# Optimization experiments

Hardware: AMD Instinct MI355X
Metric: run time of the kernel (lower is better)

The kernel has to match this reference:

```python
import jax, jax.numpy as jnp
import numpy as np

N = 100_000   # nodes
E = 3_200_000 # edges
G = 512       # graphs in batch
H = 64        # hidden dim
C = 7         # num classes


def setup_inputs() -> dict:
    key = jax.random.key(0)
    ks = jax.random.split(key, 8)
    x = jax.random.normal(ks[0], (N, 1), dtype=jnp.float32)
    edge_index = jax.random.randint(ks[1], (2, E), 0, N, dtype=jnp.int32)
    batch = jnp.sort(jax.random.randint(ks[2], (N,), 0, G, dtype=jnp.int32))
    W1 = jax.random.normal(ks[3], (1, H), dtype=jnp.float32) / np.sqrt(1.0)
    b1 = jnp.zeros((H,), jnp.float32)
    W2 = jax.random.normal(ks[4], (H, H), dtype=jnp.float32) / np.sqrt(H)
    b2 = jnp.zeros((H,), jnp.float32)
    fW1 = jax.random.normal(ks[5], (H, 32), dtype=jnp.float32) / np.sqrt(H)
    fb1 = jnp.zeros((32,), jnp.float32)
    fW2 = jax.random.normal(ks[6], (32, C), dtype=jnp.float32) / np.sqrt(32.0)
    fb2 = jnp.zeros((C,), jnp.float32)
    return {"x": x, "edge_index": edge_index, "batch": batch,
            "W1": W1, "b1": b1, "W2": W2, "b2": b2,
            "fW1": fW1, "fb1": fb1, "fW2": fW2, "fb2": fb2}


def reference(x, edge_index, batch, W1, b1, W2, b2, fW1, fb1, fW2, fb2):
    # GCNConv with self-loops and symmetric normalization (PyG defaults).
    src, dst = edge_index[0], edge_index[1]
    loop = jnp.arange(N, dtype=src.dtype)
    s = jnp.concatenate([src, loop])  # [E+N]
    d = jnp.concatenate([dst, loop])
    deg = jax.ops.segment_sum(jnp.ones(s.shape, jnp.float32), d, num_segments=N)
    dis = jnp.where(deg > 0, jax.lax.rsqrt(jnp.maximum(deg, 1.0)), 0.0)
    norm = dis[s] * dis[d]  # [E+N]

    def gcn(h, W, b):
        h = h @ W                                   # [N, out]
        msg = norm[:, None] * h[s]                  # gather + scale
        return jax.ops.segment_sum(msg, d, num_segments=N) + b

    # Dropout is identity in eval/reference mode.
    h = jax.nn.relu(gcn(x, W1, b1))
    h = jax.nn.relu(gcn(h, W2, b2))

    # global_mean_pool over graph assignment `batch`
    cnt = jax.ops.segment_sum(jnp.ones((N,), jnp.float32), batch, num_segments=G)
    pooled = jax.ops.segment_sum(h, batch, num_segments=G) / jnp.maximum(cnt, 1.0)[:, None]

    h = jax.nn.relu(pooled @ fW1 + fb1)
    return h @ fW2 + fb2  # [G, C] logits
```

## Files before the change

### kernel.cpp

```cpp
#include <hip/hip_runtime.h>

#define N_NODES 100000
#define N_EDGES 3200000
#define G_GRAPHS 512
#define HDIM 64
#define CBSH 11
#define CBN 2048
#define NCB ((N_NODES + CBN - 1) / CBN)
#define EPW 4096
#define NWG ((N_EDGES + EPW - 1) / EPW)
#define EPT (EPW / 256)
#define SPL 8
#define RTHR 512
#define WPS ((NWG + SPL - 1) / SPL)
#define MAXROWS 25

__global__ __launch_bounds__(256) void kzp(const float* __restrict__ W1,
                                           const float* __restrict__ b1,
                                           const float* __restrict__ W2,
                                           float* __restrict__ dt, int* __restrict__ meta,
                                           float* __restrict__ pw1, float* __restrict__ pb1,
                                           float* __restrict__ w2p, float* __restrict__ tabs,
                                           int* __restrict__ deg, float* __restrict__ q,
                                           float* __restrict__ pool, int* __restrict__ cnt,
                                           float* __restrict__ histA, float* __restrict__ histW) {
    int tid = threadIdx.x;
    if (blockIdx.x < 16) {
        __shared__ float ts[HDIM], srt[HDIM];
        __shared__ int isnew[HDIM], rr[HDIM], kpermS[HDIM], rankS[HDIM];
        __shared__ int ndS;
        if (tid < HDIM) {
            float w1 = W1[tid], bb = b1[tid];
            ts[tid] = (w1 != 0.f) ? (-bb / w1) : -1e30f;
        }
        __syncthreads();
        if (tid < HDIM) {
            float tj = ts[tid];
            int r = 0;
            for (int i = 0; i < HDIM; ++i) {
                float ti = ts[i];
                if (ti < tj || (ti == tj && i < tid)) r++;
            }
            rr[tid] = r;
            srt[r] = tj;
            kpermS[r] = tid;
        }
        __syncthreads();
        if (tid < HDIM) {
            int r = rr[tid];
            isnew[r] = (r == 0) || (srt[r] != srt[r - 1]);
        }
        __syncthreads();
        if (tid < HDIM) {
            int r = rr[tid];
            int didx = 0;
            for (int qq = 0; qq <= r; ++qq) didx += isnew[qq];
            didx -= 1;
            rankS[tid] = didx;
            if (blockIdx.x == 0 && isnew[r]) dt[didx] = srt[r];
        }
        if (tid == 0) {
            int nd = 0;
            for (int qq = 0; qq < HDIM; ++qq) nd += isnew[qq];
            ndS = nd;
            if (blockIdx.x == 0) {
                int nw = 0;
                for (int qq = 0; qq < HDIM; ++qq) nw |= (b1[qq] != 0.f) ? 1 : 0;
                meta[0] = nd; meta[1] = nw;
            }
        }
        __syncthreads();
        int nd = ndS;
        if (blockIdx.x == 0 && tid < HDIM) {
            int pj = kpermS[tid];
            pw1[tid] = W1[pj]; pb1[tid] = b1[pj];
        }
        int i = blockIdx.x * 256 + tid;
        if (i < HDIM * HDIM) {
            int r = i >> 6, j = i & 63;
            w2p[i] = W2[kpermS[r] * HDIM + j];
        }
        if (nd <= 6 && i < (1 + 4 * nd) * HDIM) {
            int r = i >> 6, j = i & 63;
            float acc = 0.f;
            if (r == 0) {
                for (int jj = 0; jj < HDIM; ++jj)
                    if (W1[jj] == 0.f) acc += fmaxf(b1[jj], 0.f) * W2[jj * HDIM + j];
            } else {
                int qq = (r - 1) >> 2, c = (r - 1) & 3;
                for (int jj = 0; jj < HDIM; ++jj) {
                    if (rankS[jj] != qq) continue;
                    float w1 = W1[jj], bb = b1[jj];
                    float wr = W2[jj * HDIM + j];
                    if      (c == 0 && w1 > 0.f) acc += w1 * wr;
                    else if (c == 1 && w1 < 0.f) acc += w1 * wr;
                    else if (c == 2 && w1 > 0.f) acc += bb * wr;
                    else if (c == 3 && w1 < 0.f) acc += bb * wr;
                }
            }
            tabs[i] = acc;
        }
    }
    size_t gtid = (size_t)blockIdx.x * blockDim.x + threadIdx.x;
    size_t stride = (size_t)gridDim.x * blockDim.x;
    for (size_t i = gtid; i < N_NODES; i += stride) { deg[i] = 0; q[i] = 0.f; }
    for (size_t i = gtid; i < G_GRAPHS * HDIM; i += stride) pool[i] = 0.f;
    for (size_t i = gtid; i < G_GRAPHS; i += stride) cnt[i] = 0;
    size_t nh = (size_t)7 * N_NODES;
    for (size_t i = gtid; i < nh; i += stride) { histA[i] = 0.f; histW[i] = 0.f; }
}

__global__ __launch_bounds__(256) void kB2(const int* __restrict__ src,
                                           const int* __restrict__ dst,
                                           unsigned* __restrict__ sorted,
                                           int* __restrict__ wgcnt,
                                           int* __restrict__ wgpre) {
    __shared__ int hist[NCB];
    __shared__ int basep[NCB];
    __shared__ unsigned sbuf[EPW];
    int tid = threadIdx.x;
    int w = blockIdx.x;
    int e0 = w * EPW;
    int ecnt = min(EPW, N_EDGES - e0);
    if (tid < NCB) hist[tid] = 0;
    __syncthreads();
    int dreg[EPT], sreg[EPT];
    const uint4* dst4 = reinterpret_cast<const uint4*>(dst + e0);
    const uint4* src4 = reinterpret_cast<const uint4*>(src + e0);
    #pragma unroll
    for (int t = 0; t < EPT / 4; ++t) {
        int v = t * 256 + tid;
        if (v * 4 < ecnt) {
            uint4 dv = dst4[v];
            uint4 sv = src4[v];
            int base = v * 4;
            dreg[t*4+0] = (base+0 < ecnt) ? (int)dv.x : -1;
            dreg[t*4+1] = (base+1 < ecnt) ? (int)dv.y : -1;
            dreg[t*4+2] = (base+2 < ecnt) ? (int)dv.z : -1;
            dreg[t*4+3] = (base+3 < ecnt) ? (int)dv.w : -1;
            sreg[t*4+0] = (int)sv.x; sreg[t*4+1] = (int)sv.y;
            sreg[t*4+2] = (int)sv.z; sreg[t*4+3] = (int)sv.w;
            #pragma unroll
            for (int k = 0; k < 4; ++k)
                if (dreg[t*4+k] >= 0) atomicAdd(&hist[dreg[t*4+k] >> CBSH], 1);
        } else {
            dreg[t*4+0] = dreg[t*4+1] = dreg[t*4+2] = dreg[t*4+3] = -1;
        }
    }
    __syncthreads();
    if (tid < 64) {
        int h = (tid < NCB) ? hist[tid] : 0;
        int v = h;
        #pragma unroll
        for (int off = 1; off < 64; off <<= 1) {
            int uu = __shfl_up(v, off, 64);
            if (tid >= off) v += uu;
        }
        if (tid < NCB) {
            basep[tid] = v - h;
            wgcnt[w * NCB + tid] = h;
            wgpre[w * NCB + tid] = v - h;
        }
    }
    __syncthreads();
    #pragma unroll
    for (int t = 0; t < EPT; ++t) {
        int d = dreg[t];
        if (d >= 0) {
            int b = d >> CBSH;
            int pos = atomicAdd(&basep[b], 1);
            sbuf[pos] = ((unsigned)sreg[t] << CBSH) | (unsigned)(d & (CBN - 1));
        }
    }
    __syncthreads();
    uint4* out4 = reinterpret_cast<uint4*>(sorted + e0);
    const uint4* sb4 = reinterpret_cast<const uint4*>(sbuf);
    int nv4 = ecnt >> 2;
    for (int i = tid; i < nv4; i += 256) out4[i] = sb4[i];
    for (int i = (nv4 << 2) + tid; i < ecnt; i += 256) sorted[e0 + i] = sbuf[i];
}

#define FOR_RUNS(BODY)                                                        \
    {                                                                         \
        int wv = tid >> 6, ln = tid & 63;                                     \
        int w0 = sp * WPS, w1e = min(w0 + WPS, NWG);                          \
        for (int w = w0 + wv; w < w1e; w += (RTHR / 64)) {                    \
            int st = w * EPW + wgpre[w * NCB + b];                            \
            int cb = wgcnt[w * NCB + b];                                      \
            for (int i = ln; i < cb; i += 64) { unsigned ww = sorted[st + i]; BODY } \
        }                                                                     \
    }

__global__ __launch_bounds__(RTHR) void kdeg2(const unsigned* __restrict__ sorted,
                                              const int* __restrict__ wgcnt,
                                              const int* __restrict__ wgpre,
                                              int* __restrict__ deg) {
    __shared__ int dcnt[CBN];
    int b = blockIdx.x / SPL, sp = blockIdx.x % SPL, tid = threadIdx.x;
    for (int i = tid; i < CBN; i += RTHR) dcnt[i] = 0;
    __syncthreads();
    FOR_RUNS( atomicAdd(&dcnt[ww & (CBN - 1)], 1); )
    __syncthreads();
    int nb = b * CBN;
    for (int i = tid; i < CBN; i += RTHR) {
        int c = dcnt[i];
        if (c && nb + i < N_NODES) atomicAdd(&deg[nb + i], c);
    }
}

__global__ void k2_dis(const int* __restrict__ deg, const float* __restrict__ x,
                       float* __restrict__ dis, float* __restrict__ u) {
    int n = blockIdx.x * blockDim.x + threadIdx.x;
    if (n < N_NODES) {
        float d = rsqrtf((float)(deg[n] + 1));
        dis[n] = d;
        u[n] = d * x[n];
    }
}

__global__ __launch_bounds__(RTHR) void kq3(const unsigned* __restrict__ sorted,
                                            const int* __restrict__ wgcnt,
                                            const int* __restrict__ wgpre,
                                            const float* __restrict__ u,
                                            float* __restrict__ q) {
    __shared__ float qL[CBN];
    int b = blockIdx.x / SPL, sp = blockIdx.x % SPL, tid = threadIdx.x;
    for (int i = tid; i < CBN; i += RTHR) qL[i] = 0.f;
    __syncthreads();
    FOR_RUNS( atomicAdd(&qL[ww & (CBN - 1)], u[ww >> CBSH]); )
    __syncthreads();
    int nb = b * CBN;
    for (int i = tid; i < CBN; i += RTHR) {
        float v = qL[i];
        if (v != 0.f && nb + i < N_NODES) atomicAdd(&q[nb + i], v);
    }
}

__global__ void k3b(const int* __restrict__ deg, const float* __restrict__ x,
                    const float* __restrict__ dis, const float* __restrict__ q,
                    float2* __restrict__ ad) {
    int n = blockIdx.x * blockDim.x + threadIdx.x;
    if (n < N_NODES) {
        float d = dis[n];
        ad[n] = make_float2(d * q[n] + x[n] / (float)(deg[n] + 1), d);
    }
}

__global__ __launch_bounds__(RTHR) void khist(const unsigned* __restrict__ sorted,
                                              const int* __restrict__ wgcnt,
                                              const int* __restrict__ wgpre,
                                              const float2* __restrict__ ad,
                                              const float* __restrict__ dt,
                                              const int* __restrict__ meta,
                                              float* __restrict__ histA,
                                              float* __restrict__ histW) {
    __shared__ float bA[7 * CBN];
    __shared__ float dtS[8];
    int nd = meta[0], needW = meta[1];
    if (nd > 6) return;
    int b = blockIdx.x / SPL, sp = blockIdx.x % SPL, tid = threadIdx.x;
    if (tid < 8) dtS[tid] = (tid < nd) ? dt[tid] : 3.4e38f;
    int nb = b * CBN;
    int nparts = 1 + (needW ? 1 : 0);
    for (int part = 0; part < nparts; ++part) {
        for (int i = tid; i < (nd + 1) * CBN; i += RTHR) bA[i] = 0.f;
        __syncthreads();
        FOR_RUNS(
            float2 t = ad[ww >> CBSH];
            float a = t.x;
            int k = 0;
            _Pragma("unroll")
            for (int qq = 0; qq < 6; ++qq) k += (dtS[qq] < a) ? 1 : 0;
            atomicAdd(&bA[k * CBN + (ww & (CBN - 1))], part ? t.y : t.y * a);
        )
        __syncthreads();
        float* H = part ? histW : histA;
        for (int k = 0; k <= nd; ++k)
            for (int i = tid; i < CBN; i += RTHR) {
                float v = bA[k * CBN + i];
                if (v != 0.f && nb + i < N_NODES)
                    atomicAdd(&H[(size_t)k * N_NODES + nb + i], v);
            }
        __syncthreads();
    }
}

__global__ __launch_bounds__(256) void knode(
        const float* __restrict__ histA, const float* __restrict__ histW,
        const int* __restrict__ meta, const float* __restrict__ dt,
        const float* __restrict__ tabs,
        const float* __restrict__ pw1, const float* __restrict__ pb1,
        const float* __restrict__ w2p,
        const float2* __restrict__ ad, const float* __restrict__ b2,
        const int* __restrict__ batch,
        const unsigned* __restrict__ sorted, const int* __restrict__ wgcnt,
        const int* __restrict__ wgpre,
        float* __restrict__ pool, int* __restrict__ cnt) {
    __shared__ float h2s[HDIM * 65];
    __shared__ float tabL[MAXROWS * HDIM];
    __shared__ float dtS[8];
    int tid = threadIdx.x;
    int nl = tid & 63, cg = tid >> 6;
    int n0 = blockIdx.x * 64;
    int nvalid = min(64, N_NODES - n0);
    int n = n0 + min(nl, nvalid - 1);
    int nd = meta[0], needW = meta[1];
    float2 adn = ad[n];
    float a = adn.x, d = adn.y;
    int c16 = cg * 16;

    if (nd <= 6) {
        int nrows = 1 + 4 * nd;
        for (int i = tid; i < nrows * HDIM; i += 256) tabL[i] = tabs[i];
        if (tid < nd) dtS[tid] = dt[tid];
        __syncthreads();
        float TA = 0.f, TW = 0.f;
        for (int bq = 0; bq <= nd; ++bq) {
            TA += histA[(size_t)bq * N_NODES + n];
            if (needW) TW += histW[(size_t)bq * N_NODES + n];
        }
        int k = 0;
        for (int q = 0; q < nd; ++q) k += (dtS[q] < a) ? 1 : 0;
        float z[16];
        #pragma unroll
        for (int t = 0; t < 16; ++t) z[t] = b2[c16 + t];
        float d2 = d * d;
        float cC = d * TW + d2;
        #pragma unroll
        for (int t = 0; t < 16; ++t) z[t] += cC * tabL[c16 + t];
        float run = 0.f, runW = 0.f;
        for (int q = 0; q < nd; ++q) {
            run += histA[(size_t)q * N_NODES + n];
            if (needW) runW += histW[(size_t)q * N_NODES + n];
            bool act = (q < k);
            float cWp = d * (TA - run) + (act ? d2 * a : 0.f);
            float cWm = d * run + (act ? 0.f : d2 * a);
            float cBp = d * (TW - runW) + (act ? d2 : 0.f);
            float cBm = d * runW + (act ? 0.f : d2);
            int base = (1 + 4 * q) * HDIM + c16;
            #pragma unroll
            for (int t = 0; t < 16; ++t)
                z[t] += cWp * tabL[base + t] + cWm * tabL[base + HDIM + t]
                      + cBp * tabL[base + 2 * HDIM + t] + cBm * tabL[base + 3 * HDIM + t];
        }
        #pragma unroll
        for (int t = 0; t < 16; ++t) h2s[nl * 65 + c16 + t] = fmaxf(z[t], 0.f);
    } else {
        float zz[16];
        #pragma unroll
        for (int t = 0; t < 16; ++t) zz[t] = 0.f;
        int b = n >> CBSH;
        int myld = n & (CBN - 1);
        for (int w = 0; w < NWG; ++w) {
            int st = w * EPW + wgpre[w * NCB + b];
            int cb = wgcnt[w * NCB + b];
            for (int i = 0; i < cb; ++i) {
                unsigned ww = sorted[st + i];
                if ((int)(ww & (CBN - 1)) == myld) {
                    float2 t2 = ad[ww >> CBSH];
                    #pragma unroll
                    for (int t = 0; t < 16; ++t)
                        zz[t] += t2.y * fmaxf(t2.x * pw1[c16 + t] + pb1[c16 + t], 0.f);
                }
            }
        }
        #pragma unroll
        for (int t = 0; t < 16; ++t)
            zz[t] = d * zz[t] + d * d * fmaxf(a * pw1[c16 + t] + pb1[c16 + t], 0.f);
        #pragma unroll
        for (int t = 0; t < 16; ++t) h2s[nl * 65 + c16 + t] = zz[t];
        __syncthreads();
        float z[16];
        #pragma unroll
        for (int t = 0; t < 16; ++t) z[t] = b2[c16 + t];
        for (int jj = 0; jj < HDIM; ++jj) {
            float av = h2s[nl * 65 + jj];
            #pragma unroll
            for (int t = 0; t < 16; ++t) z[t] += av * w2p[jj * HDIM + c16 + t];
        }
        __syncthreads();
        #pragma unroll
        for (int t = 0; t < 16; ++t) h2s[nl * 65 + c16 + t] = fmaxf(z[t], 0.f);
    }

    __syncthreads();
    int i0 = cg * 16, i1 = min(i0 + 16, nvalid);
    float accP = 0.f; int gcur = -1, runC = 0;
    for (int i = i0; i < i1; ++i) {
        int g = batch[n0 + i];
        float v = h2s[i * 65 + nl];
        if (g != gcur) {
            if (gcur >= 0) {
                atomicAdd(&pool[(size_t)gcur * HDIM + nl], accP);
                if (nl == 0) atomicAdd(&cnt[gcur], runC);
            }
            gcur = g; accP = 0.f; runC = 0;
        }
        accP += v; ++runC;
    }
    if (gcur >= 0) {
        atomicAdd(&pool[(size_t)gcur * HDIM + nl], accP);
        if (nl == 0) atomicAdd(&cnt[gcur], runC);
    }
}

__global__ void k7_mlp(const float* __restrict__ pool, const int* __restrict__ cnt,
                       const float* __restrict__ fW1, const float* __restrict__ fb1,
                       const float* __restrict__ fW2, const float* __restrict__ fb2,
                       float* __restrict__ out) {
    __shared__ float p[HDIM];
    __shared__ float tt[32];
    int g = blockIdx.x;
    int tid = threadIdx.x;
    float c = fmaxf((float)cnt[g], 1.f);
    p[tid] = pool[g * HDIM + tid] / c;
    __syncthreads();
    if (tid < 32) {
        float acc = fb1[tid];
        #pragma unroll
        for (int j = 0; j < HDIM; ++j) acc += p[j] * fW1[j * 32 + tid];
        tt[tid] = fmaxf(acc, 0.f);
    }
    __syncthreads();
    if (tid < 7) {
        float acc = fb2[tid];
        #pragma unroll
        for (int i = 0; i < 32; ++i) acc += tt[i] * fW2[i * 7 + tid];
        out[g * 7 + tid] = acc;
    }
}

__global__ void kf1_deg(const int* __restrict__ dst, int* __restrict__ deg) {
    int e = blockIdx.x * blockDim.x + threadIdx.x;
    if (e < N_EDGES) atomicAdd(&deg[dst[e]], 1);
}
__global__ void kf2_dis(const int* __restrict__ deg, const float* __restrict__ x,
                        float* __restrict__ dis, float* __restrict__ agg1) {
    int n = blockIdx.x * blockDim.x + threadIdx.x;
    if (n < N_NODES) {
        float d = (float)(deg[n] + 1);
        dis[n] = rsqrtf(d);
        agg1[n] = x[n] / d;
    }
}
__global__ void kf3_agg1(const int* __restrict__ src, const int* __restrict__ dst,
                         const float* __restrict__ dis, const float* __restrict__ x,
                         float* __restrict__ agg1) {
    int e = blockIdx.x * blockDim.x + threadIdx.x;
    if (e < N_EDGES) {
        int s = src[e], d = dst[e];
        atomicAdd(&agg1[d], dis[s] * dis[d] * x[s]);
    }
}
__global__ void kf4_agg2init(const float* __restrict__ agg1, const float* __restrict__ dis,
                             const float* __restrict__ W1, const float* __restrict__ b1,
                             float* __restrict__ agg2) {
    int i = blockIdx.x * blockDim.x + threadIdx.x;
    if (i < N_NODES * HDIM) {
        int n = i >> 6, j = i & 63;
        float h = fmaxf(agg1[n] * W1[j] + b1[j], 0.f);
        float r = dis[n];
        agg2[i] = r * r * h;
    }
}
__global__ void kf5_edge(const int* __restrict__ src, const int* __restrict__ dst,
                         const float* __restrict__ dis, const float* __restrict__ agg1,
                         const float* __restrict__ W1, const float* __restrict__ b1,
                         float* __restrict__ agg2) {
    int t = blockIdx.x * blockDim.x + threadIdx.x;
    int e = t >> 6, j = t & 63;
    if (e < N_EDGES) {
        int s = src[e], d = dst[e];
        float w = dis[s] * dis[d];
        float h = fmaxf(agg1[s] * W1[j] + b1[j], 0.f);
        atomicAdd(&agg2[d * HDIM + j], w * h);
    }
}
__global__ void kf6_pool(const float* __restrict__ agg2, const float* __restrict__ W2,
                         const float* __restrict__ b2, const int* __restrict__ batch,
                         float* __restrict__ pool, int* __restrict__ cnt) {
    __shared__ float w2s[HDIM * HDIM];
    int tid = threadIdx.x;
    for (int i = tid; i < HDIM * HDIM; i += blockDim.x) w2s[i] = W2[i];
    __syncthreads();
    int lane = tid & 63, wid = tid >> 6;
    int nwaves = gridDim.x * 4;
    for (int n = blockIdx.x * 4 + wid; n < N_NODES; n += nwaves) {
        float av  = agg2[n * HDIM + lane];
        float acc = b2[lane];
        #pragma unroll
        for (int k = 0; k < HDIM; ++k)
            acc += __shfl(av, k, 64) * w2s[k * HDIM + lane];
        acc = fmaxf(acc, 0.f);
        int g = batch[n];
        atomicAdd(&pool[g * HDIM + lane], acc);
        if (lane == 0) atomicAdd(&cnt[g], 1);
    }
}

extern "C" void kernel_launch(void* const* d_in, const int* in_sizes, int n_in,
                              void* d_out, int out_size, void* d_ws, size_t ws_size,
                              hipStream_t stream) {
    const float* x    = (const float*)d_in[0];
    const int*   ei   = (const int*)  d_in[1];
    const int*   batch= (const int*)  d_in[2];
    const float* W1   = (const float*)d_in[3];
    const float* b1   = (const float*)d_in[4];
    const float* W2   = (const float*)d_in[5];
    const float* b2   = (const float*)d_in[6];
    const float* fW1  = (const float*)d_in[7];
    const float* fb1  = (const float*)d_in[8];
    const float* fW2  = (const float*)d_in[9];
    const float* fb2  = (const float*)d_in[10];
    const int* src = ei;
    const int* dst = ei + N_EDGES;
    float* out = (float*)d_out;

    size_t off = 0;
    auto take = [&](size_t bytes) { size_t o = off; off = (off + bytes + 255) & ~(size_t)255; return o; };
    char* base = (char*)d_ws;
    int*     deg   = (int*)     (base + take((size_t)N_NODES * 4));
    float*   pool  = (float*)   (base + take((size_t)G_GRAPHS * HDIM * 4));
    int*     cnt   = (int*)     (base + take((size_t)G_GRAPHS * 4));
    float*   dis   = (float*)   (base + take((size_t)N_NODES * 4));
    float*   u     = (float*)   (base + take((size_t)N_NODES * 4));
    float*   q     = (float*)   (base + take((size_t)N_NODES * 4));
    float2*  ad    = (float2*)  (base + take((size_t)N_NODES * 8));
    float*   dt    = (float*)   (base + take(HDIM * 4));
    int*     meta  = (int*)     (base + take(64));
    float*   pw1   = (float*)   (base + take(HDIM * 4));
    float*   pb1   = (float*)   (base + take(HDIM * 4));
    float*   w2p   = (float*)   (base + take(HDIM * HDIM * 4));
    float*   tabs  = (float*)   (base + take((size_t)MAXROWS * HDIM * 4));
    int*     wgcnt = (int*)     (base + take((size_t)NWG * NCB * 4));
    int*     wgpre = (int*)     (base + take((size_t)NWG * NCB * 4));
    size_t sorted_off = off;
    unsigned* sorted = (unsigned*)(base + take((size_t)N_EDGES * 4));
    float*   histA = (float*)   (base + take((size_t)7 * N_NODES * 4));
    float*   histW = (float*)   (base + take((size_t)7 * N_NODES * 4));
    size_t need_fast = off;

    if (ws_size >= need_fast) {
        kzp   <<<1024, 256, 0, stream>>>(W1, b1, W2, dt, meta, pw1, pb1, w2p, tabs,
                                         deg, q, pool, cnt, histA, histW);
        kB2   <<<NWG, 256, 0, stream>>>(src, dst, sorted, wgcnt, wgpre);
        kdeg2 <<<NCB * SPL, RTHR, 0, stream>>>(sorted, wgcnt, wgpre, deg);
        k2_dis<<<(N_NODES + 255) / 256, 256, 0, stream>>>(deg, x, dis, u);
        kq3   <<<NCB * SPL, RTHR, 0, stream>>>(sorted, wgcnt, wgpre, u, q);
        k3b   <<<(N_NODES + 255) / 256, 256, 0, stream>>>(deg, x, dis, q, ad);
        khist <<<NCB * SPL, RTHR, 0, stream>>>(sorted, wgcnt, wgpre, ad, dt, meta, histA, histW);
        knode <<<(N_NODES + 63) / 64, 256, 0, stream>>>(histA, histW, meta, dt, tabs,
                                                        pw1, pb1, w2p, ad, b2, batch,
                                                        sorted, wgcnt, wgpre, pool, cnt);
        k7_mlp<<<G_GRAPHS, 64, 0, stream>>>(pool, cnt, fW1, fb1, fW2, fb2, out);
    } else {
        float* agg1 = u;
        float* agg2 = (float*)(base + sorted_off);
        hipMemsetAsync(deg, 0, (size_t)N_NODES * 4, stream);
        hipMemsetAsync(pool, 0, (size_t)G_GRAPHS * HDIM * 4 + 1024, stream);
        kf1_deg<<<(N_EDGES + 255) / 256, 256, 0, stream>>>(dst, deg);
        kf2_dis<<<(N_NODES + 255) / 256, 256, 0, stream>>>(deg, x, dis, agg1);
        kf3_agg1<<<(N_EDGES + 255) / 256, 256, 0, stream>>>(src, dst, dis, x, agg1);
        kf4_agg2init<<<(N_NODES * HDIM + 255) / 256, 256, 0, stream>>>(agg1, dis, W1, b1, agg2);
        int k5_blocks = (int)(((long long)N_EDGES * HDIM + 255) / 256);
        kf5_edge<<<k5_blocks, 256, 0, stream>>>(src, dst, dis, agg1, W1, b1, agg2);
        kf6_pool<<<2048, 256, 0, stream>>>(agg2, W2, b2, batch, pool, cnt);
        k7_mlp<<<G_GRAPHS, 64, 0, stream>>>(pool, cnt, fW1, fb1, fW2, fb2, out);
    }
}
```

Measured before the change: 134.0 us.

## Merge bucket-sort and zero/prep kernels; recompute node scalars in consumers

Folds the edge bucketing kernel and the zero-init/weight-prep kernel into one launch by partitioning block indices. It also removes two small elementwise kernels (dis/u and ad computation) by recomputing rsqrt(deg+1) and the node scalar inline in the gather loops. This cuts launch count and intermediate buffer traffic. In exchange the consumers do extra gathers (deg, x, q instead of one float2) and an rsqrt per edge.

```diff
diff --git a/kernel.cpp b/kernel.cpp
--- a/kernel.cpp
+++ b/kernel.cpp
@@ -14,8 +14,14 @@
 #define RTHR 512
 #define WPS ((NWG + SPL - 1) / SPL)
 #define MAXROWS 25
-
-__global__ __launch_bounds__(256) void kzp(const float* __restrict__ W1,
+#define ZBLK 1024
+
+__global__ __launch_bounds__(256) void kBZ(const int* __restrict__ src,
+                                           const int* __restrict__ dst,
+                                           unsigned* __restrict__ sorted,
+                                           int* __restrict__ wgcnt,
+                                           int* __restrict__ wgpre,
+                                           const float* __restrict__ W1,
                                            const float* __restrict__ b1,
                                            const float* __restrict__ W2,
                                            float* __restrict__ dt, int* __restrict__ meta,
@@ -25,7 +31,73 @@
                                            float* __restrict__ pool, int* __restrict__ cnt,
                                            float* __restrict__ histA, float* __restrict__ histW) {
     int tid = threadIdx.x;
-    if (blockIdx.x < 16) {
+    if (blockIdx.x < NWG) {
+        __shared__ int hist[NCB];
+        __shared__ int basep[NCB];
+        __shared__ unsigned sbuf[EPW];
+        int w = blockIdx.x;
+        int e0 = w * EPW;
+        int ecnt = min(EPW, N_EDGES - e0);
+        if (tid < NCB) hist[tid] = 0;
+        __syncthreads();
+        int dreg[EPT], sreg[EPT];
+        const uint4* dst4 = reinterpret_cast<const uint4*>(dst + e0);
+        const uint4* src4 = reinterpret_cast<const uint4*>(src + e0);
+        #pragma unroll
+        for (int t = 0; t < EPT / 4; ++t) {
+            int v = t * 256 + tid;
+            if (v * 4 < ecnt) {
+                uint4 dv = dst4[v];
+                uint4 sv = src4[v];
+                int base = v * 4;
+                dreg[t*4+0] = (base+0 < ecnt) ? (int)dv.x : -1;
+                dreg[t*4+1] = (base+1 < ecnt) ? (int)dv.y : -1;
+                dreg[t*4+2] = (base+2 < ecnt) ? (int)dv.z : -1;
+                dreg[t*4+3] = (base+3 < ecnt) ? (int)dv.w : -1;
+                sreg[t*4+0] = (int)sv.x; sreg[t*4+1] = (int)sv.y;
+                sreg[t*4+2] = (int)sv.z; sreg[t*4+3] = (int)sv.w;
+                #pragma unroll
+                for (int k = 0; k < 4; ++k)
+                    if (dreg[t*4+k] >= 0) atomicAdd(&hist[dreg[t*4+k] >> CBSH], 1);
+            } else {
+                dreg[t*4+0] = dreg[t*4+1] = dreg[t*4+2] = dreg[t*4+3] = -1;
+            }
+        }
+        __syncthreads();
+        if (tid < 64) {
+            int h = (tid < NCB) ? hist[tid] : 0;
+            int v = h;
+            #pragma unroll
+            for (int off = 1; off < 64; off <<= 1) {
+                int uu = __shfl_up(v, off, 64);
+                if (tid >= off) v += uu;
+            }
+            if (tid < NCB) {
+                basep[tid] = v - h;
+                wgcnt[w * NCB + tid] = h;
+                wgpre[w * NCB + tid] = v - h;
+            }
+        }
+        __syncthreads();
+        #pragma unroll
+        for (int t = 0; t < EPT; ++t) {
+            int d = dreg[t];
+            if (d >= 0) {
+                int b = d >> CBSH;
+                int pos = atomicAdd(&basep[b], 1);
+                sbuf[pos] = ((unsigned)sreg[t] << CBSH) | (unsigned)(d & (CBN - 1));
+            }
+        }
+        __syncthreads();
+        uint4* out4 = reinterpret_cast<uint4*>(sorted + e0);
+        const uint4* sb4 = reinterpret_cast<const uint4*>(sbuf);
+        int nv4 = ecnt >> 2;
+        for (int i = tid; i < nv4; i += 256) out4[i] = sb4[i];
+        for (int i = (nv4 << 2) + tid; i < ecnt; i += 256) sorted[e0 + i] = sbuf[i];
+        return;
+    }
+    int zb = blockIdx.x - NWG;
+    if (zb < 16) {
         __shared__ float ts[HDIM], srt[HDIM];
         __shared__ int isnew[HDIM], rr[HDIM], kpermS[HDIM], rankS[HDIM];
         __shared__ int ndS;
@@ -57,13 +129,13 @@
             for (int qq = 0; qq <= r; ++qq) didx += isnew[qq];
             didx -= 1;
             rankS[tid] = didx;
-            if (blockIdx.x == 0 && isnew[r]) dt[didx] = srt[r];
+            if (zb == 0 && isnew[r]) dt[didx] = srt[r];
         }
         if (tid == 0) {
             int nd = 0;
             for (int qq = 0; qq < HDIM; ++qq) nd += isnew[qq];
             ndS = nd;
-            if (blockIdx.x == 0) {
+            if (zb == 0) {
                 int nw = 0;
                 for (int qq = 0; qq < HDIM; ++qq) nw |= (b1[qq] != 0.f) ? 1 : 0;
                 meta[0] = nd; meta[1] = nw;
@@ -71,11 +143,11 @@
         }
         __syncthreads();
         int nd = ndS;
-        if (blockIdx.x == 0 && tid < HDIM) {
+        if (zb == 0 && tid < HDIM) {
             int pj = kpermS[tid];
             pw1[tid] = W1[pj]; pb1[tid] = b1[pj];
         }
-        int i = blockIdx.x * 256 + tid;
+        int i = zb * 256 + tid;
         if (i < HDIM * HDIM) {
             int r = i >> 6, j = i & 63;
             w2p[i] = W2[kpermS[r] * HDIM + j];
@@ -101,83 +173,13 @@
             tabs[i] = acc;
         }
     }
-    size_t gtid = (size_t)blockIdx.x * blockDim.x + threadIdx.x;
-    size_t stride = (size_t)gridDim.x * blockDim.x;
+    size_t gtid = (size_t)zb * 256 + tid;
+    size_t stride = (size_t)ZBLK * 256;
     for (size_t i = gtid; i < N_NODES; i += stride) { deg[i] = 0; q[i] = 0.f; }
     for (size_t i = gtid; i < G_GRAPHS * HDIM; i += stride) pool[i] = 0.f;
     for (size_t i = gtid; i < G_GRAPHS; i += stride) cnt[i] = 0;
     size_t nh = (size_t)7 * N_NODES;
     for (size_t i = gtid; i < nh; i += stride) { histA[i] = 0.f; histW[i] = 0.f; }
-}
-
-__global__ __launch_bounds__(256) void kB2(const int* __restrict__ src,
-                                           const int* __restrict__ dst,
-                                           unsigned* __restrict__ sorted,
-                                           int* __restrict__ wgcnt,
-                                           int* __restrict__ wgpre) {
-    __shared__ int hist[NCB];
-    __shared__ int basep[NCB];
-    __shared__ unsigned sbuf[EPW];
-    int tid = threadIdx.x;
-    int w = blockIdx.x;
-    int e0 = w * EPW;
-    int ecnt = min(EPW, N_EDGES - e0);
-    if (tid < NCB) hist[tid] = 0;
-    __syncthreads();
-    int dreg[EPT], sreg[EPT];
-    const uint4* dst4 = reinterpret_cast<const uint4*>(dst + e0);
-    const uint4* src4 = reinterpret_cast<const uint4*>(src + e0);
-    #pragma unroll
-    for (int t = 0; t < EPT / 4; ++t) {
-        int v = t * 256 + tid;
-        if (v * 4 < ecnt) {
-            uint4 dv = dst4[v];
-            uint4 sv = src4[v];
-            int base = v * 4;
-            dreg[t*4+0] = (base+0 < ecnt) ? (int)dv.x : -1;
-            dreg[t*4+1] = (base+1 < ecnt) ? (int)dv.y : -1;
-            dreg[t*4+2] = (base+2 < ecnt) ? (int)dv.z : -1;
-            dreg[t*4+3] = (base+3 < ecnt) ? (int)dv.w : -1;
-            sreg[t*4+0] = (int)sv.x; sreg[t*4+1] = (int)sv.y;
-            sreg[t*4+2] = (int)sv.z; sreg[t*4+3] = (int)sv.w;
-            #pragma unroll
-            for (int k = 0; k < 4; ++k)
-                if (dreg[t*4+k] >= 0) atomicAdd(&hist[dreg[t*4+k] >> CBSH], 1);
-        } else {
-            dreg[t*4+0] = dreg[t*4+1] = dreg[t*4+2] = dreg[t*4+3] = -1;
-        }
-    }
-    __syncthreads();
-    if (tid < 64) {
-        int h = (tid < NCB) ? hist[tid] : 0;
-        int v = h;
-        #pragma unroll
-        for (int off = 1; off < 64; off <<= 1) {
-            int uu = __shfl_up(v, off, 64);
-            if (tid >= off) v += uu;
-        }
-        if (tid < NCB) {
-            basep[tid] = v - h;
-            wgcnt[w * NCB + tid] = h;
-            wgpre[w * NCB + tid] = v - h;
-        }
-    }
-    __syncthreads();
-    #pragma unroll
-    for (int t = 0; t < EPT; ++t) {
-        int d = dreg[t];
-        if (d >= 0) {
-            int b = d >> CBSH;
-            int pos = atomicAdd(&basep[b], 1);
-            sbuf[pos] = ((unsigned)sreg[t] << CBSH) | (unsigned)(d & (CBN - 1));
-        }
-    }
-    __syncthreads();
-    uint4* out4 = reinterpret_cast<uint4*>(sorted + e0);
-    const uint4* sb4 = reinterpret_cast<const uint4*>(sbuf);
-    int nv4 = ecnt >> 2;
-    for (int i = tid; i < nv4; i += 256) out4[i] = sb4[i];
-    for (int i = (nv4 << 2) + tid; i < ecnt; i += 256) sorted[e0 + i] = sbuf[i];
 }
 
 #define FOR_RUNS(BODY)                                                        \
@@ -208,26 +210,21 @@
     }
 }
 
-__global__ void k2_dis(const int* __restrict__ deg, const float* __restrict__ x,
-                       float* __restrict__ dis, float* __restrict__ u) {
-    int n = blockIdx.x * blockDim.x + threadIdx.x;
-    if (n < N_NODES) {
-        float d = rsqrtf((float)(deg[n] + 1));
-        dis[n] = d;
-        u[n] = d * x[n];
-    }
-}
-
 __global__ __launch_bounds__(RTHR) void kq3(const unsigned* __restrict__ sorted,
                                             const int* __restrict__ wgcnt,
                                             const int* __restrict__ wgpre,
-                                            const float* __restrict__ u,
+                                            const int* __restrict__ deg,
+                                            const float* __restrict__ x,
                                             float* __restrict__ q) {
     __shared__ float qL[CBN];
     int b = blockIdx.x / SPL, sp = blockIdx.x % SPL, tid = threadIdx.x;
     for (int i = tid; i < CBN; i += RTHR) qL[i] = 0.f;
     __syncthreads();
-    FOR_RUNS( atomicAdd(&qL[ww & (CBN - 1)], u[ww >> CBSH]); )
+    FOR_RUNS(
+        int s = ww >> CBSH;
+        float dn = rsqrtf((float)(deg[s] + 1));
+        atomicAdd(&qL[ww & (CBN - 1)], dn * x[s]);
+    )
     __syncthreads();
     int nb = b * CBN;
     for (int i = tid; i < CBN; i += RTHR) {
@@ -236,20 +233,12 @@
     }
 }
 
-__global__ void k3b(const int* __restrict__ deg, const float* __restrict__ x,
-                    const float* __restrict__ dis, const float* __restrict__ q,
-                    float2* __restrict__ ad) {
-    int n = blockIdx.x * blockDim.x + threadIdx.x;
-    if (n < N_NODES) {
-        float d = dis[n];
-        ad[n] = make_float2(d * q[n] + x[n] / (float)(deg[n] + 1), d);
-    }
-}
-
 __global__ __launch_bounds__(RTHR) void khist(const unsigned* __restrict__ sorted,
                                               const int* __restrict__ wgcnt,
                                               const int* __restrict__ wgpre,
-                                              const float2* __restrict__ ad,
+                                              const float* __restrict__ q,
+                                              const int* __restrict__ deg,
+                                              const float* __restrict__ x,
                                               const float* __restrict__ dt,
                                               const int* __restrict__ meta,
                                               float* __restrict__ histA,
@@ -266,12 +255,13 @@
         for (int i = tid; i < (nd + 1) * CBN; i += RTHR) bA[i] = 0.f;
         __syncthreads();
         FOR_RUNS(
-            float2 t = ad[ww >> CBSH];
-            float a = t.x;
+            int s = ww >> CBSH;
+            float dn = rsqrtf((float)(deg[s] + 1));
+            float a = dn * q[s] + x[s] * dn * dn;
             int k = 0;
             _Pragma("unroll")
             for (int qq = 0; qq < 6; ++qq) k += (dtS[qq] < a) ? 1 : 0;
-            atomicAdd(&bA[k * CBN + (ww & (CBN - 1))], part ? t.y : t.y * a);
+            atomicAdd(&bA[k * CBN + (ww & (CBN - 1))], part ? dn : dn * a);
         )
         __syncthreads();
         float* H = part ? histW : histA;
@@ -291,7 +281,8 @@
         const float* __restrict__ tabs,
         const float* __restrict__ pw1, const float* __restrict__ pb1,
         const float* __restrict__ w2p,
-        const float2* __restrict__ ad, const float* __restrict__ b2,
+        const float* __restrict__ q, const int* __restrict__ deg,
+        const float* __restrict__ x, const float* __restrict__ b2,
         const int* __restrict__ batch,
         const unsigned* __restrict__ sorted, const int* __restrict__ wgcnt,
         const int* __restrict__ wgpre,
@@ -305,8 +296,8 @@
     int nvalid = min(64, N_NODES - n0);
     int n = n0 + min(nl, nvalid - 1);
     int nd = meta[0], needW = meta[1];
-    float2 adn = ad[n];
-    float a = adn.x, d = adn.y;
+    float d = rsqrtf((float)(deg[n] + 1));
+    float a = d * q[n] + x[n] * d * d;
     int c16 = cg * 16;
 
     if (nd <= 6) {
@@ -320,7 +311,7 @@
             if (needW) TW += histW[(size_t)bq * N_NODES + n];
         }
         int k = 0;
-        for (int q = 0; q < nd; ++q) k += (dtS[q] < a) ? 1 : 0;
+        for (int qq = 0; qq < nd; ++qq) k += (dtS[qq] < a) ? 1 : 0;
         float z[16];
         #pragma unroll
         for (int t = 0; t < 16; ++t) z[t] = b2[c16 + t];
@@ -329,15 +320,15 @@
         #pragma unroll
         for (int t = 0; t < 16; ++t) z[t] += cC * tabL[c16 + t];
         float run = 0.f, runW = 0.f;
-        for (int q = 0; q < nd; ++q) {
-            run += histA[(size_t)q * N_NODES + n];
-            if (needW) runW += histW[(size_t)q * N_NODES + n];
-            bool act = (q < k);
+        for (int qq = 0; qq < nd; ++qq) {
+            run += histA[(size_t)qq * N_NODES + n];
+            if (needW) runW += histW[(size_t)qq * N_NODES + n];
+            bool act = (qq < k);
             float cWp = d * (TA - run) + (act ? d2 * a : 0.f);
             float cWm = d * run + (act ? 0.f : d2 * a);
             float cBp = d * (TW - runW) + (act ? d2 : 0.f);
             float cBm = d * runW + (act ? 0.f : d2);
-            int base = (1 + 4 * q) * HDIM + c16;
+            int base = (1 + 4 * qq) * HDIM + c16;
             #pragma unroll
             for (int t = 0; t < 16; ++t)
                 z[t] += cWp * tabL[base + t] + cWm * tabL[base + HDIM + t]
@@ -357,10 +348,12 @@
             for (int i = 0; i < cb; ++i) {
                 unsigned ww = sorted[st + i];
                 if ((int)(ww & (CBN - 1)) == myld) {
-                    float2 t2 = ad[ww >> CBSH];
+                    int s2 = (int)(ww >> CBSH);
+                    float dn2 = rsqrtf((float)(deg[s2] + 1));
+                    float a2 = dn2 * q[s2] + x[s2] * dn2 * dn2;
                     #pragma unroll
                     for (int t = 0; t < 16; ++t)
-                        zz[t] += t2.y * fmaxf(t2.x * pw1[c16 + t] + pb1[c16 + t], 0.f);
+                        zz[t] += dn2 * fmaxf(a2 * pw1[c16 + t] + pb1[c16 + t], 0.f);
                 }
             }
         }
@@ -525,7 +518,6 @@
     float*   dis   = (float*)   (base + take((size_t)N_NODES * 4));
     float*   u     = (float*)   (base + take((size_t)N_NODES * 4));
     float*   q     = (float*)   (base + take((size_t)N_NODES * 4));
-    float2*  ad    = (float2*)  (base + take((size_t)N_NODES * 8));
     float*   dt    = (float*)   (base + take(HDIM * 4));
     int*     meta  = (int*)     (base + take(64));
     float*   pw1   = (float*)   (base + take(HDIM * 4));
@@ -541,16 +533,15 @@
     size_t need_fast = off;
 
     if (ws_size >= need_fast) {
-        kzp   <<<1024, 256, 0, stream>>>(W1, b1, W2, dt, meta, pw1, pb1, w2p, tabs,
-                                         deg, q, pool, cnt, histA, histW);
-        kB2   <<<NWG, 256, 0, stream>>>(src, dst, sorted, wgcnt, wgpre);
+        kBZ   <<<NWG + ZBLK, 256, 0, stream>>>(src, dst, sorted, wgcnt, wgpre,
+                                               W1, b1, W2, dt, meta, pw1, pb1, w2p, tabs,
+                                               deg, q, pool, cnt, histA, histW);
         kdeg2 <<<NCB * SPL, RTHR, 0, stream>>>(sorted, wgcnt, wgpre, deg);
-        k2_dis<<<(N_NODES + 255) / 256, 256, 0, stream>>>(deg, x, dis, u);
-        kq3   <<<NCB * SPL, RTHR, 0, stream>>>(sorted, wgcnt, wgpre, u, q);
-        k3b   <<<(N_NODES + 255) / 256, 256, 0, stream>>>(deg, x, dis, q, ad);
-        khist <<<NCB * SPL, RTHR, 0, stream>>>(sorted, wgcnt, wgpre, ad, dt, meta, histA, histW);
+        kq3   <<<NCB * SPL, RTHR, 0, stream>>>(sorted, wgcnt, wgpre, deg, x, q);
+        khist <<<NCB * SPL, RTHR, 0, stream>>>(sorted, wgcnt, wgpre, q, deg, x, dt, meta,
+                                               histA, histW);
         knode <<<(N_NODES + 63) / 64, 256, 0, stream>>>(histA, histW, meta, dt, tabs,
-                                                        pw1, pb1, w2p, ad, b2, batch,
+                                                        pw1, pb1, w2p, q, deg, x, b2, batch,
                                                         sorted, wgcnt, wgpre, pool, cnt);
         k7_mlp<<<G_GRAPHS, 64, 0, stream>>>(pool, cnt, fW1, fb1, fW2, fb2, out);
     } else {
```

New measurement: 150.3 us. +12.1%, slower.
